# Kernel optimization log

Measured on AMD Instinct MI355X. Metric: run time of the kernel, lower is better.

## Reference

```python
import jax, jax.numpy as jnp
import numpy as np

B, N, D, H, C = 2048, 6, 2048, 1024, 200  # batch, nodes/graph, feat dim, hidden, classes
ALPHA = 0.015   # distance decay in edge weight
SCALE = 24.0    # weight rescale after mean-subtraction + clamp


def setup_inputs() -> dict:
    key = jax.random.key(0)
    k1, k2, k3, k4 = jax.random.split(key, 4)
    part_feats = jax.random.normal(k1, (B, N, D), dtype=jnp.float32)
    # cdds columns: [score, y0, x0, y1, x1, idx]; only cols 1:5 (box coords) are used
    cdds = jax.random.uniform(k2, (B, N, 6), dtype=jnp.float32) * 448.0
    fc_w = jax.random.normal(k3, (2 * D, H), dtype=jnp.float32) * 0.02
    fc_b = jnp.zeros((H,), dtype=jnp.float32)
    cls_w = jax.random.normal(k4, (H, C), dtype=jnp.float32) * 0.02
    cls_b = jnp.zeros((C,), dtype=jnp.float32)
    return {"part_feats": part_feats, "cdds": cdds, "fc_w": fc_w, "fc_b": fc_b,
            "cls_w": cls_w, "cls_b": cls_b}


def reference(part_feats, cdds, fc_w, fc_b, cls_w, cls_b):
    # --- edge weights on per-sample complete graph (apply_edges) ---
    loc = cdds[:, :, 1:5]                      # (B, N, 4) = (y0, x0, y1, x1)
    cy = (loc[..., 0] + loc[..., 2]) * 0.5     # node center y, (B, N)
    cx = (loc[..., 1] + loc[..., 3]) * 0.5     # node center x, (B, N)
    dx = cx[:, :, None] - cx[:, None, :]       # (B, N, N) pairwise
    dy = cy[:, :, None] - cy[:, None, :]
    d2 = dx * dx + dy * dy
    mask = ~jnp.eye(N, dtype=bool)             # off-diagonal = real edges (30 per graph)
    dist = jnp.sqrt(jnp.where(mask, d2, 1.0))  # safe sqrt off the diagonal
    w0 = jnp.where(mask, jnp.exp(-ALPHA * dist), 0.0)
    mean_w = jnp.sum(w0, axis=(1, 2), keepdims=True) / (N * (N - 1))  # mean over 30 edges
    w = SCALE * jnp.maximum(w0 - mean_w, 0.0) * mask                  # (B, N, N), w[b,u,v]
    # --- update_all: u_mul_e + mean over the (N-1) incoming edges per node ---
    hidden = jnp.einsum('buv,bud->bvd', w, part_feats) / (N - 1)      # (B, N, D)
    # --- node MLP + graph mean readout + classifier ---
    node_ft = jnp.concatenate([hidden, part_feats], axis=-1) @ fc_w + fc_b  # (B, N, H)
    g_ft = node_ft.mean(axis=1)                                             # (B, H)
    return g_ft @ cls_w + cls_b                                             # (B, C)
```

## Files before the change

kernel.cpp:

```cpp
#include <hip/hip_runtime.h>
#include <math.h>

namespace {
constexpr int NB = 2048;
constexpr int NNODE = 6;
constexpr int DD = 2048;
constexpr int HH = 1024;
constexpr int CC = 200;
constexpr int K2 = 2 * DD;
constexpr int NPAD = 256;
constexpr int ZS1 = 4;
constexpr int ZS2 = 16;
constexpr float ALPHA_C = 0.015f;
constexpr float SCALE_C = 24.0f;
}

typedef __attribute__((ext_vector_type(8))) short bf16x8;
typedef __attribute__((ext_vector_type(4))) float f32x4;

static __device__ __forceinline__ unsigned short f2bf(float x) {
    union { float f; unsigned int u; } v; v.f = x;
    unsigned int r = v.u + 0x7FFFu + ((v.u >> 16) & 1u);
    return (unsigned short)(r >> 16);
}

static __device__ __forceinline__ void compute_s_wave(const float* __restrict__ cdds,
                                                      int b, float sv[NNODE]) {
    const int lane = threadIdx.x & 63;
    const int u = lane >> 3;
    const int v = lane & 7;
    const float* cd = cdds + (size_t)b * 36;
    float w = 0.f;
    const bool valid = (u < 6) & (v < 6) & (u != v);
    if (u < 6 && v < 6 && u != v) {
        float cyu = (cd[u * 6 + 1] + cd[u * 6 + 3]) * 0.5f;
        float cxu = (cd[u * 6 + 2] + cd[u * 6 + 4]) * 0.5f;
        float cyv = (cd[v * 6 + 1] + cd[v * 6 + 3]) * 0.5f;
        float cxv = (cd[v * 6 + 2] + cd[v * 6 + 4]) * 0.5f;
        float dx = cxu - cxv, dy = cyu - cyv;
        w = expf(-ALPHA_C * sqrtf(dx * dx + dy * dy));
    }
    float s = w;
#pragma unroll
    for (int m = 32; m >= 1; m >>= 1) s += __shfl_xor(s, m);
    float mean = s * (1.f / 30.f);
    float tt = valid ? fmaxf(w - mean, 0.f) : 0.f;
    tt += __shfl_xor(tt, 1);
    tt += __shfl_xor(tt, 2);
    tt += __shfl_xor(tt, 4);
    float su = SCALE_C * tt * 0.2f;
#pragma unroll
    for (int uu = 0; uu < NNODE; ++uu) sv[uu] = __shfl(su, uu * 8);
}

__global__ __launch_bounds__(256) void k_cvt(const float* __restrict__ cls_w,
                                             unsigned short* __restrict__ cls_wT)
{
    __shared__ float sm[64 * 65];
    const int kt = blockIdx.x & 15;
    const int nt = blockIdx.x >> 4;
    const int t = threadIdx.x;
#pragma unroll
    for (int c = 0; c < 4; ++c) {
        int i = t + c * 256;
        int kr = i >> 4;
        int n4 = (i & 15) << 2;
        int gn = nt * 64 + n4;
        const float* sp = cls_w + (size_t)(kt * 64 + kr) * CC + gn;
        float4 v = {0.f, 0.f, 0.f, 0.f};
        if (gn + 3 < CC) {
            v = *(const float4*)sp;
        } else {
            if (gn + 0 < CC) v.x = sp[0];
            if (gn + 1 < CC) v.y = sp[1];
            if (gn + 2 < CC) v.z = sp[2];
            if (gn + 3 < CC) v.w = sp[3];
        }
        sm[kr * 65 + n4 + 0] = v.x; sm[kr * 65 + n4 + 1] = v.y;
        sm[kr * 65 + n4 + 2] = v.z; sm[kr * 65 + n4 + 3] = v.w;
    }
    __syncthreads();
#pragma unroll
    for (int c = 0; c < 4; ++c) {
        int i = t + c * 256;
        int nr = i >> 4;
        int k4 = (i & 15) << 2;
        ushort4 o;
        o.x = f2bf(sm[(k4 + 0) * 65 + nr]);
        o.y = f2bf(sm[(k4 + 1) * 65 + nr]);
        o.z = f2bf(sm[(k4 + 2) * 65 + nr]);
        o.w = f2bf(sm[(k4 + 3) * 65 + nr]);
        *(ushort4*)(cls_wT + (size_t)(nt * 64 + nr) * HH + kt * 64 + k4) = o;
    }
}

__global__ __launch_bounds__(256) void k_g1(const float* __restrict__ fc_w,
                                            const unsigned short* __restrict__ Bt,
                                            float* __restrict__ partM)
{
    __shared__ short As[32][72];
    __shared__ short Bs[256][72];
    const int t = threadIdx.x;
    const int lane = t & 63;
    const int wid = t >> 6;
    const int bm = blockIdx.x * 32;
    const int z = blockIdx.y;
    const int kbase = z * (HH / ZS1);

    f32x4 acc[2][4] = {};

    for (int k0 = kbase; k0 < kbase + HH / ZS1; k0 += 64) {
#pragma unroll
        for (int c = 0; c < 2; ++c) {
            int i = t + c * 256;
            int row = i >> 4;
            int k4 = (i & 15) << 2;
            float4 v = *(const float4*)(fc_w + (size_t)(bm + row) * HH + k0 + k4);
            ushort4 o;
            o.x = f2bf(v.x); o.y = f2bf(v.y); o.z = f2bf(v.z); o.w = f2bf(v.w);
            *(ushort4*)&As[row][k4] = o;
        }
#pragma unroll
        for (int c = 0; c < 8; ++c) {
            int i = t + c * 256;
            int n = i >> 3;
            int k8 = (i & 7) << 3;
            *(uint4*)&Bs[n][k8] =
                *(const uint4*)(Bt + (size_t)n * HH + k0 + k8);
        }
        __syncthreads();
#pragma unroll
        for (int ks = 0; ks < 2; ++ks) {
            int kk = ks * 32 + ((lane >> 4) << 3);
            int ar = lane & 15;
            bf16x8 a0 = *(const bf16x8*)&As[ar][kk];
            bf16x8 a1 = *(const bf16x8*)&As[16 + ar][kk];
#pragma unroll
            for (int fn = 0; fn < 4; ++fn) {
                bf16x8 b = *(const bf16x8*)&Bs[wid * 64 + fn * 16 + ar][kk];
                acc[0][fn] = __builtin_amdgcn_mfma_f32_16x16x32_bf16(a0, b, acc[0][fn], 0, 0, 0);
                acc[1][fn] = __builtin_amdgcn_mfma_f32_16x16x32_bf16(a1, b, acc[1][fn], 0, 0, 0);
            }
        }
        __syncthreads();
    }
#pragma unroll
    for (int fm = 0; fm < 2; ++fm)
#pragma unroll
        for (int fn = 0; fn < 4; ++fn) {
            int gm0 = bm + fm * 16 + ((lane >> 4) << 2);
            int gn = wid * 64 + fn * 16 + (lane & 15);
#pragma unroll
            for (int r = 0; r < 4; ++r)
                partM[((size_t)z * K2 + gm0 + r) * NPAD + gn] = acc[fm][fn][r];
        }
}

__global__ __launch_bounds__(256) void k_red(const float* __restrict__ partM,
                                             const float* __restrict__ cls_w,
                                             const float* __restrict__ fc_b,
                                             const float* __restrict__ cls_b,
                                             unsigned short* __restrict__ Mt,
                                             float* __restrict__ bvec)
{
    __shared__ float sm[64][69];
    __shared__ float red[256];
    const int bx = blockIdx.x;
    const int t = threadIdx.x;

    if (bx >= 256) {
        const int bb = bx - 256;
        int c8 = t & 7;
        int hs = t >> 3;
        int c = bb * 8 + c8;
        float acc = 0.f;
        for (int h = hs; h < HH; h += 32)
            acc += fc_b[h] * cls_w[(size_t)h * CC + c];
        red[t] = acc;
        __syncthreads();
        for (int s = 128; s >= 8; s >>= 1) {
            if (t < s) red[t] += red[t + s];
            __syncthreads();
        }
        if (t < 8) bvec[c] = red[t] + cls_b[c];
        return;
    }

    const int bm = (bx >> 2) * 64;
    const int bn = (bx & 3) * 64;
#pragma unroll
    for (int c = 0; c < 4; ++c) {
        int i = t + c * 256;
        int mr = i >> 4;
        int n4 = (i & 15) << 2;
        float4 s = {0.f, 0.f, 0.f, 0.f};
#pragma unroll
        for (int z = 0; z < ZS1; ++z) {
            float4 v = *(const float4*)(partM +
                ((size_t)z * K2 + bm + mr) * NPAD + bn + n4);
            s.x += v.x; s.y += v.y; s.z += v.z; s.w += v.w;
        }
        sm[mr][n4 + 0] = s.x; sm[mr][n4 + 1] = s.y;
        sm[mr][n4 + 2] = s.z; sm[mr][n4 + 3] = s.w;
    }
    __syncthreads();
#pragma unroll
    for (int c = 0; c < 4; ++c) {
        int i = t + c * 256;
        int nr = i >> 4;
        int m4 = (i & 15) << 2;
        ushort4 o;
        o.x = f2bf(sm[m4 + 0][nr]);
        o.y = f2bf(sm[m4 + 1][nr]);
        o.z = f2bf(sm[m4 + 2][nr]);
        o.w = f2bf(sm[m4 + 3][nr]);
        *(ushort4*)(Mt + (size_t)(bn + nr) * K2 + bm + m4) = o;
    }
}

__global__ __launch_bounds__(256) void k_pq(const float* __restrict__ pf,
                                            const float* __restrict__ cdds,
                                            unsigned short* __restrict__ pq)
{
    const int bid = blockIdx.x;
    const int b = bid >> 1;
    const int d = ((bid & 1) << 10) + (threadIdx.x << 2);

    const float* base = pf + (size_t)b * NNODE * DD + d;
    float4 v0 = *(const float4*)(base + 0 * DD);
    float4 v1 = *(const float4*)(base + 1 * DD);
    float4 v2 = *(const float4*)(base + 2 * DD);
    float4 v3 = *(const float4*)(base + 3 * DD);
    float4 v4 = *(const float4*)(base + 4 * DD);
    float4 v5 = *(const float4*)(base + 5 * DD);

    float sv[NNODE];
    compute_s_wave(cdds, b, sv);

    float4 q;
    q.x = v0.x + v1.x + v2.x + v3.x + v4.x + v5.x;
    q.y = v0.y + v1.y + v2.y + v3.y + v4.y + v5.y;
    q.z = v0.z + v1.z + v2.z + v3.z + v4.z + v5.z;
    q.w = v0.w + v1.w + v2.w + v3.w + v4.w + v5.w;

    float4 p = {0.f, 0.f, 0.f, 0.f};
    p.x = fmaf(sv[0], v0.x, p.x); p.y = fmaf(sv[0], v0.y, p.y);
    p.z = fmaf(sv[0], v0.z, p.z); p.w = fmaf(sv[0], v0.w, p.w);
    p.x = fmaf(sv[1], v1.x, p.x); p.y = fmaf(sv[1], v1.y, p.y);
    p.z = fmaf(sv[1], v1.z, p.z); p.w = fmaf(sv[1], v1.w, p.w);
    p.x = fmaf(sv[2], v2.x, p.x); p.y = fmaf(sv[2], v2.y, p.y);
    p.z = fmaf(sv[2], v2.z, p.z); p.w = fmaf(sv[2], v2.w, p.w);
    p.x = fmaf(sv[3], v3.x, p.x); p.y = fmaf(sv[3], v3.y, p.y);
    p.z = fmaf(sv[3], v3.z, p.z); p.w = fmaf(sv[3], v3.w, p.w);
    p.x = fmaf(sv[4], v4.x, p.x); p.y = fmaf(sv[4], v4.y, p.y);
    p.z = fmaf(sv[4], v4.z, p.z); p.w = fmaf(sv[4], v4.w, p.w);
    p.x = fmaf(sv[5], v5.x, p.x); p.y = fmaf(sv[5], v5.y, p.y);
    p.z = fmaf(sv[5], v5.z, p.z); p.w = fmaf(sv[5], v5.w, p.w);

    unsigned short* o = pq + (size_t)b * K2;
    ushort4 pb, qb;
    pb.x = f2bf(p.x); pb.y = f2bf(p.y); pb.z = f2bf(p.z); pb.w = f2bf(p.w);
    qb.x = f2bf(q.x); qb.y = f2bf(q.y); qb.z = f2bf(q.z); qb.w = f2bf(q.w);
    *(ushort4*)(o + d) = pb;
    *(ushort4*)(o + DD + d) = qb;
}

__global__ __launch_bounds__(256) void k_gemm2(const unsigned short* __restrict__ A,
                                               const unsigned short* __restrict__ Bt,
                                               float* __restrict__ part)
{
    __shared__ short As[64][72];
    __shared__ short Bs[256][72];
    const int t = threadIdx.x;
    const int lane = t & 63;
    const int wid = t >> 6;
    const int wr = wid >> 1, wc = wid & 1;
    const int bm = blockIdx.x * 64;
    const int z = blockIdx.y;
    const int kbase = z * (K2 / ZS2);

    f32x4 acc[2][8] = {};

    for (int k0 = kbase; k0 < kbase + K2 / ZS2; k0 += 64) {
#pragma unroll
        for (int c = 0; c < 2; ++c) {
            int i = t + c * 256;
            int row = i >> 3;
            int k8 = (i & 7) << 3;
            *(uint4*)&As[row][k8] =
                *(const uint4*)(A + (size_t)(bm + row) * K2 + k0 + k8);
        }
#pragma unroll
        for (int c = 0; c < 8; ++c) {
            int i = t + c * 256;
            int n = i >> 3;
            int k8 = (i & 7) << 3;
            *(uint4*)&Bs[n][k8] =
                *(const uint4*)(Bt + (size_t)n * K2 + k0 + k8);
        }
        __syncthreads();
#pragma unroll
        for (int ks = 0; ks < 2; ++ks) {
            int kk = ks * 32 + ((lane >> 4) << 3);
            int ar = lane & 15;
            bf16x8 a0 = *(const bf16x8*)&As[wr * 32 + ar][kk];
            bf16x8 a1 = *(const bf16x8*)&As[wr * 32 + 16 + ar][kk];
#pragma unroll
            for (int fn = 0; fn < 8; ++fn) {
                bf16x8 b = *(const bf16x8*)&Bs[wc * 128 + fn * 16 + ar][kk];
                acc[0][fn] = __builtin_amdgcn_mfma_f32_16x16x32_bf16(a0, b, acc[0][fn], 0, 0, 0);
                acc[1][fn] = __builtin_amdgcn_mfma_f32_16x16x32_bf16(a1, b, acc[1][fn], 0, 0, 0);
            }
        }
        __syncthreads();
    }
#pragma unroll
    for (int fm = 0; fm < 2; ++fm)
#pragma unroll
        for (int fn = 0; fn < 8; ++fn) {
            int gm0 = bm + wr * 32 + fm * 16 + ((lane >> 4) << 2);
            int gn = wc * 128 + fn * 16 + (lane & 15);
#pragma unroll
            for (int r = 0; r < 4; ++r)
                part[((size_t)z * NB + gm0 + r) * NPAD + gn] = acc[fm][fn][r];
        }
}

__global__ __launch_bounds__(256) void k_combine(const float* __restrict__ part,
                                                 const float* __restrict__ bvec,
                                                 float* __restrict__ out)
{
    int idx = blockIdx.x * blockDim.x + threadIdx.x;
    if (idx >= NB * CC) return;
    int b = idx / CC;
    int c = idx - b * CC;
    float s = 0.f;
#pragma unroll
    for (int z = 0; z < ZS2; ++z)
        s += part[((size_t)z * NB + b) * NPAD + c];
    out[idx] = s * (1.f / 6.f) + bvec[c];
}

extern "C" void kernel_launch(void* const* d_in, const int* in_sizes, int n_in,
                              void* d_out, int out_size, void* d_ws, size_t ws_size,
                              hipStream_t stream)
{
    const float* part_feats = (const float*)d_in[0];
    const float* cdds = (const float*)d_in[1];
    const float* fc_w = (const float*)d_in[2];
    const float* fc_b = (const float*)d_in[3];
    const float* cls_w = (const float*)d_in[4];
    const float* cls_b = (const float*)d_in[5];
    float* out = (float*)d_out;

    char* ws = (char*)d_ws;
    size_t off = 0;
    unsigned short* pq = (unsigned short*)(ws + off);     off += (size_t)NB * K2 * 2;
    unsigned short* Mt = (unsigned short*)(ws + off);     off += (size_t)NPAD * K2 * 2;
    unsigned short* cls_wT = (unsigned short*)(ws + off); off += (size_t)NPAD * HH * 2;
    float* partM = (float*)(ws + off);                    off += (size_t)ZS1 * K2 * NPAD * 4;
    float* part = (float*)(ws + off);                     off += (size_t)ZS2 * NB * NPAD * 4;
    float* bvec = (float*)(ws + off);                     off += 256 * 4;

    k_cvt<<<dim3(64), dim3(256), 0, stream>>>(cls_w, cls_wT);
    k_pq<<<dim3(NB * 2), dim3(256), 0, stream>>>(part_feats, cdds, pq);
    k_g1<<<dim3(K2 / 32, ZS1), dim3(256), 0, stream>>>(fc_w, cls_wT, partM);
    k_red<<<dim3(256 + 25), dim3(256), 0, stream>>>(partM, cls_w, fc_b, cls_b, Mt, bvec);
    k_gemm2<<<dim3(NB / 64, ZS2), dim3(256), 0, stream>>>(pq, Mt, part);
    k_combine<<<dim3((NB * CC + 255) / 256), dim3(256), 0, stream>>>(part, bvec, out);
}
```

Measured before the change: 69.33 us.

## Merge independent kernels, store split-K partials in bf16, retile gemm2 warps

Folds the bias-vector computation into the cls_w conversion kernel and runs the pq feature-reduction blocks in the same launch as the first GEMM. This cuts launch count and lets independent work overlap. The second GEMM's split-K partials are now stored as bf16 instead of fp32, halving that write/read traffic, and the combine kernel reads them vectorized four at a time. The gemm2 warp tiling changes from a 2x2 warp grid to four warps each covering all 64 rows by 64 columns, which reuses the A fragments across more MFMAs. Rounding each of 16 partials to bf16 adds accuracy error.

Measured after the change: 69.93 us. Within noise of the previous version (+0.9%).

```diff
diff --git a/kernel.cpp b/kernel.cpp
--- a/kernel.cpp
+++ b/kernel.cpp
@@ -13,6 +13,8 @@
 constexpr int ZS2 = 16;
 constexpr float ALPHA_C = 0.015f;
 constexpr float SCALE_C = 24.0f;
+
+constexpr int G1_BLOCKS = (K2 / 32) * ZS1;
 }
 
 typedef __attribute__((ext_vector_type(8))) short bf16x8;
@@ -22,6 +24,11 @@
     union { float f; unsigned int u; } v; v.f = x;
     unsigned int r = v.u + 0x7FFFu + ((v.u >> 16) & 1u);
     return (unsigned short)(r >> 16);
+}
+
+static __device__ __forceinline__ float bf2f(unsigned short u) {
+    union { unsigned int i; float f; } v; v.i = ((unsigned int)u) << 16;
+    return v.f;
 }
 
 static __device__ __forceinline__ void compute_s_wave(const float* __restrict__ cdds,
@@ -53,13 +60,35 @@
     for (int uu = 0; uu < NNODE; ++uu) sv[uu] = __shfl(su, uu * 8);
 }
 
-__global__ __launch_bounds__(256) void k_cvt(const float* __restrict__ cls_w,
-                                             unsigned short* __restrict__ cls_wT)
+__global__ __launch_bounds__(256) void k_small(const float* __restrict__ cls_w,
+                                               const float* __restrict__ fc_b,
+                                               const float* __restrict__ cls_b,
+                                               unsigned short* __restrict__ cls_wT,
+                                               float* __restrict__ bvec)
 {
     __shared__ float sm[64 * 65];
-    const int kt = blockIdx.x & 15;
-    const int nt = blockIdx.x >> 4;
+    const int bx = blockIdx.x;
     const int t = threadIdx.x;
+    if (bx >= 64) {
+        const int bb = bx - 64;
+        float* red = sm;
+        int c8 = t & 7;
+        int hs = t >> 3;
+        int c = bb * 8 + c8;
+        float acc = 0.f;
+        for (int h = hs; h < HH; h += 32)
+            acc += fc_b[h] * cls_w[(size_t)h * CC + c];
+        red[t] = acc;
+        __syncthreads();
+        for (int s = 128; s >= 8; s >>= 1) {
+            if (t < s) red[t] += red[t + s];
+            __syncthreads();
+        }
+        if (t < 8) bvec[c] = red[t] + cls_b[c];
+        return;
+    }
+    const int kt = bx & 15;
+    const int nt = bx >> 4;
 #pragma unroll
     for (int c = 0; c < 4; ++c) {
         int i = t + c * 256;
@@ -94,17 +123,66 @@
     }
 }
 
-__global__ __launch_bounds__(256) void k_g1(const float* __restrict__ fc_w,
-                                            const unsigned short* __restrict__ Bt,
-                                            float* __restrict__ partM)
+__global__ __launch_bounds__(256) void k_mid(const float* __restrict__ pf,
+                                             const float* __restrict__ cdds,
+                                             const float* __restrict__ fc_w,
+                                             const unsigned short* __restrict__ Bt,
+                                             unsigned short* __restrict__ pq,
+                                             float* __restrict__ partM)
 {
     __shared__ short As[32][72];
     __shared__ short Bs[256][72];
+    const int bx = blockIdx.x;
     const int t = threadIdx.x;
+
+    if (bx >= G1_BLOCKS) {
+        const int bid = bx - G1_BLOCKS;
+        const int b = bid >> 1;
+        const int d = ((bid & 1) << 10) + (t << 2);
+        const float* base = pf + (size_t)b * NNODE * DD + d;
+        float4 v0 = *(const float4*)(base + 0 * DD);
+        float4 v1 = *(const float4*)(base + 1 * DD);
+        float4 v2 = *(const float4*)(base + 2 * DD);
+        float4 v3 = *(const float4*)(base + 3 * DD);
+        float4 v4 = *(const float4*)(base + 4 * DD);
+        float4 v5 = *(const float4*)(base + 5 * DD);
+
+        float sv[NNODE];
+        compute_s_wave(cdds, b, sv);
+
+        float4 q;
+        q.x = v0.x + v1.x + v2.x + v3.x + v4.x + v5.x;
+        q.y = v0.y + v1.y + v2.y + v3.y + v4.y + v5.y;
+        q.z = v0.z + v1.z + v2.z + v3.z + v4.z + v5.z;
+        q.w = v0.w + v1.w + v2.w + v3.w + v4.w + v5.w;
+
+        float4 p = {0.f, 0.f, 0.f, 0.f};
+        p.x = fmaf(sv[0], v0.x, p.x); p.y = fmaf(sv[0], v0.y, p.y);
+        p.z = fmaf(sv[0], v0.z, p.z); p.w = fmaf(sv[0], v0.w, p.w);
+        p.x = fmaf(sv[1], v1.x, p.x); p.y = fmaf(sv[1], v1.y, p.y);
+        p.z = fmaf(sv[1], v1.z, p.z); p.w = fmaf(sv[1], v1.w, p.w);
+        p.x = fmaf(sv[2], v2.x, p.x); p.y = fmaf(sv[2], v2.y, p.y);
+        p.z = fmaf(sv[2], v2.z, p.z); p.w = fmaf(sv[2], v2.w, p.w);
+        p.x = fmaf(sv[3], v3.x, p.x); p.y = fmaf(sv[3], v3.y, p.y);
+        p.z = fmaf(sv[3], v3.z, p.z); p.w = fmaf(sv[3], v3.w, p.w);
+        p.x = fmaf(sv[4], v4.x, p.x); p.y = fmaf(sv[4], v4.y, p.y);
+        p.z = fmaf(sv[4], v4.z, p.z); p.w = fmaf(sv[4], v4.w, p.w);
+        p.x = fmaf(sv[5], v5.x, p.x); p.y = fmaf(sv[5], v5.y, p.y);
+        p.z = fmaf(sv[5], v5.z, p.z); p.w = fmaf(sv[5], v5.w, p.w);
+
+        unsigned short* o = pq + (size_t)b * K2;
+        ushort4 pb, qb;
+        pb.x = f2bf(p.x); pb.y = f2bf(p.y); pb.z = f2bf(p.z); pb.w = f2bf(p.w);
+        qb.x = f2bf(q.x); qb.y = f2bf(q.y); qb.z = f2bf(q.z); qb.w = f2bf(q.w);
+        *(ushort4*)(o + d) = pb;
+        *(ushort4*)(o + DD + d) = qb;
+        return;
+    }
+
     const int lane = t & 63;
     const int wid = t >> 6;
-    const int bm = blockIdx.x * 32;
-    const int z = blockIdx.y;
+    const int bm = (bx >> 2) * 32;
+    const int z = bx & 3;
     const int kbase = z * (HH / ZS1);
 
     f32x4 acc[2][4] = {};
@@ -157,35 +235,11 @@
 }
 
 __global__ __launch_bounds__(256) void k_red(const float* __restrict__ partM,
-                                             const float* __restrict__ cls_w,
-                                             const float* __restrict__ fc_b,
-                                             const float* __restrict__ cls_b,
-                                             unsigned short* __restrict__ Mt,
-                                             float* __restrict__ bvec)
+                                             unsigned short* __restrict__ Mt)
 {
     __shared__ float sm[64][69];
-    __shared__ float red[256];
     const int bx = blockIdx.x;
     const int t = threadIdx.x;
-
-    if (bx >= 256) {
-        const int bb = bx - 256;
-        int c8 = t & 7;
-        int hs = t >> 3;
-        int c = bb * 8 + c8;
-        float acc = 0.f;
-        for (int h = hs; h < HH; h += 32)
-            acc += fc_b[h] * cls_w[(size_t)h * CC + c];
-        red[t] = acc;
-        __syncthreads();
-        for (int s = 128; s >= 8; s >>= 1) {
-            if (t < s) red[t] += red[t + s];
-            __syncthreads();
-        }
-        if (t < 8) bvec[c] = red[t] + cls_b[c];
-        return;
-    }
-
     const int bm = (bx >> 2) * 64;
     const int bn = (bx & 3) * 64;
 #pragma unroll
@@ -218,68 +272,20 @@
     }
 }
 
-__global__ __launch_bounds__(256) void k_pq(const float* __restrict__ pf,
-                                            const float* __restrict__ cdds,
-                                            unsigned short* __restrict__ pq)
-{
-    const int bid = blockIdx.x;
-    const int b = bid >> 1;
-    const int d = ((bid & 1) << 10) + (threadIdx.x << 2);
-
-    const float* base = pf + (size_t)b * NNODE * DD + d;
-    float4 v0 = *(const float4*)(base + 0 * DD);
-    float4 v1 = *(const float4*)(base + 1 * DD);
-    float4 v2 = *(const float4*)(base + 2 * DD);
-    float4 v3 = *(const float4*)(base + 3 * DD);
-    float4 v4 = *(const float4*)(base + 4 * DD);
-    float4 v5 = *(const float4*)(base + 5 * DD);
-
-    float sv[NNODE];
-    compute_s_wave(cdds, b, sv);
-
-    float4 q;
-    q.x = v0.x + v1.x + v2.x + v3.x + v4.x + v5.x;
-    q.y = v0.y + v1.y + v2.y + v3.y + v4.y + v5.y;
-    q.z = v0.z + v1.z + v2.z + v3.z + v4.z + v5.z;
-    q.w = v0.w + v1.w + v2.w + v3.w + v4.w + v5.w;
-
-    float4 p = {0.f, 0.f, 0.f, 0.f};
-    p.x = fmaf(sv[0], v0.x, p.x); p.y = fmaf(sv[0], v0.y, p.y);
-    p.z = fmaf(sv[0], v0.z, p.z); p.w = fmaf(sv[0], v0.w, p.w);
-    p.x = fmaf(sv[1], v1.x, p.x); p.y = fmaf(sv[1], v1.y, p.y);
-    p.z = fmaf(sv[1], v1.z, p.z); p.w = fmaf(sv[1], v1.w, p.w);
-    p.x = fmaf(sv[2], v2.x, p.x); p.y = fmaf(sv[2], v2.y, p.y);
-    p.z = fmaf(sv[2], v2.z, p.z); p.w = fmaf(sv[2], v2.w, p.w);
-    p.x = fmaf(sv[3], v3.x, p.x); p.y = fmaf(sv[3], v3.y, p.y);
-    p.z = fmaf(sv[3], v3.z, p.z); p.w = fmaf(sv[3], v3.w, p.w);
-    p.x = fmaf(sv[4], v4.x, p.x); p.y = fmaf(sv[4], v4.y, p.y);
-    p.z = fmaf(sv[4], v4.z, p.z); p.w = fmaf(sv[4], v4.w, p.w);
-    p.x = fmaf(sv[5], v5.x, p.x); p.y = fmaf(sv[5], v5.y, p.y);
-    p.z = fmaf(sv[5], v5.z, p.z); p.w = fmaf(sv[5], v5.w, p.w);
-
-    unsigned short* o = pq + (size_t)b * K2;
-    ushort4 pb, qb;
-    pb.x = f2bf(p.x); pb.y = f2bf(p.y); pb.z = f2bf(p.z); pb.w = f2bf(p.w);
-    qb.x = f2bf(q.x); qb.y = f2bf(q.y); qb.z = f2bf(q.z); qb.w = f2bf(q.w);
-    *(ushort4*)(o + d) = pb;
-    *(ushort4*)(o + DD + d) = qb;
-}
-
 __global__ __launch_bounds__(256) void k_gemm2(const unsigned short* __restrict__ A,
                                                const unsigned short* __restrict__ Bt,
-                                               float* __restrict__ part)
+                                               unsigned short* __restrict__ part)
 {
     __shared__ short As[64][72];
     __shared__ short Bs[256][72];
     const int t = threadIdx.x;
     const int lane = t & 63;
     const int wid = t >> 6;
-    const int wr = wid >> 1, wc = wid & 1;
     const int bm = blockIdx.x * 64;
     const int z = blockIdx.y;
     const int kbase = z * (K2 / ZS2);
 
-    f32x4 acc[2][8] = {};
+    f32x4 acc[4][4] = {};
 
     for (int k0 = kbase; k0 < kbase + K2 / ZS2; k0 += 64) {
 #pragma unroll
@@ -303,42 +309,53 @@
         for (int ks = 0; ks < 2; ++ks) {
             int kk = ks * 32 + ((lane >> 4) << 3);
             int ar = lane & 15;
-            bf16x8 a0 = *(const bf16x8*)&As[wr * 32 + ar][kk];
-            bf16x8 a1 = *(const bf16x8*)&As[wr * 32 + 16 + ar][kk];
-#pragma unroll
-            for (int fn = 0; fn < 8; ++fn) {
-                bf16x8 b = *(const bf16x8*)&Bs[wc * 128 + fn * 16 + ar][kk];
+            bf16x8 a0 = *(const bf16x8*)&As[0 * 16 + ar][kk];
+            bf16x8 a1 = *(const bf16x8*)&As[1 * 16 + ar][kk];
+            bf16x8 a2 = *(const bf16x8*)&As[2 * 16 + ar][kk];
+            bf16x8 a3 = *(const bf16x8*)&As[3 * 16 + ar][kk];
+#pragma unroll
+            for (int fn = 0; fn < 4; ++fn) {
+                bf16x8 b = *(const bf16x8*)&Bs[wid * 64 + fn * 16 + ar][kk];
                 acc[0][fn] = __builtin_amdgcn_mfma_f32_16x16x32_bf16(a0, b, acc[0][fn], 0, 0, 0);
                 acc[1][fn] = __builtin_amdgcn_mfma_f32_16x16x32_bf16(a1, b, acc[1][fn], 0, 0, 0);
+                acc[2][fn] = __builtin_amdgcn_mfma_f32_16x16x32_bf16(a2, b, acc[2][fn], 0, 0, 0);
+                acc[3][fn] = __builtin_amdgcn_mfma_f32_16x16x32_bf16(a3, b, acc[3][fn], 0, 0, 0);
             }
         }
         __syncthreads();
     }
 #pragma unroll
-    for (int fm = 0; fm < 2; ++fm)
-#pragma unroll
-        for (int fn = 0; fn < 8; ++fn) {
-            int gm0 = bm + wr * 32 + fm * 16 + ((lane >> 4) << 2);
-            int gn = wc * 128 + fn * 16 + (lane & 15);
+    for (int fm = 0; fm < 4; ++fm)
+#pragma unroll
+        for (int fn = 0; fn < 4; ++fn) {
+            int gm0 = bm + fm * 16 + ((lane >> 4) << 2);
+            int gn = wid * 64 + fn * 16 + (lane & 15);
 #pragma unroll
             for (int r = 0; r < 4; ++r)
-                part[((size_t)z * NB + gm0 + r) * NPAD + gn] = acc[fm][fn][r];
-        }
-}
-
-__global__ __launch_bounds__(256) void k_combine(const float* __restrict__ part,
+                part[((size_t)z * NB + gm0 + r) * NPAD + gn] = f2bf(acc[fm][fn][r]);
+        }
+}
+
+__global__ __launch_bounds__(256) void k_combine(const unsigned short* __restrict__ part,
                                                  const float* __restrict__ bvec,
                                                  float* __restrict__ out)
 {
     int idx = blockIdx.x * blockDim.x + threadIdx.x;
-    if (idx >= NB * CC) return;
-    int b = idx / CC;
-    int c = idx - b * CC;
-    float s = 0.f;
-#pragma unroll
-    for (int z = 0; z < ZS2; ++z)
-        s += part[((size_t)z * NB + b) * NPAD + c];
-    out[idx] = s * (1.f / 6.f) + bvec[c];
+    if (idx >= NB * (CC / 4)) return;
+    int b = idx / (CC / 4);
+    int c0 = (idx - b * (CC / 4)) << 2;
+    float s0 = 0.f, s1 = 0.f, s2 = 0.f, s3 = 0.f;
+#pragma unroll
+    for (int z = 0; z < ZS2; ++z) {
+        ushort4 v = *(const ushort4*)(part + ((size_t)z * NB + b) * NPAD + c0);
+        s0 += bf2f(v.x); s1 += bf2f(v.y); s2 += bf2f(v.z); s3 += bf2f(v.w);
+    }
+    float4 o;
+    o.x = s0 * (1.f / 6.f) + bvec[c0 + 0];
+    o.y = s1 * (1.f / 6.f) + bvec[c0 + 1];
+    o.z = s2 * (1.f / 6.f) + bvec[c0 + 2];
+    o.w = s3 * (1.f / 6.f) + bvec[c0 + 3];
+    *(float4*)(out + (size_t)b * CC + c0) = o;
 }
 
 extern "C" void kernel_launch(void* const* d_in, const int* in_sizes, int n_in,
@@ -359,13 +376,13 @@
     unsigned short* Mt = (unsigned short*)(ws + off);     off += (size_t)NPAD * K2 * 2;
     unsigned short* cls_wT = (unsigned short*)(ws + off); off += (size_t)NPAD * HH * 2;
     float* partM = (float*)(ws + off);                    off += (size_t)ZS1 * K2 * NPAD * 4;
-    float* part = (float*)(ws + off);                     off += (size_t)ZS2 * NB * NPAD * 4;
+    unsigned short* part = (unsigned short*)(ws + off);   off += (size_t)ZS2 * NB * NPAD * 2;
     float* bvec = (float*)(ws + off);                     off += 256 * 4;
 
-    k_cvt<<<dim3(64), dim3(256), 0, stream>>>(cls_w, cls_wT);
-    k_pq<<<dim3(NB * 2), dim3(256), 0, stream>>>(part_feats, cdds, pq);
-    k_g1<<<dim3(K2 / 32, ZS1), dim3(256), 0, stream>>>(fc_w, cls_wT, partM);
-    k_red<<<dim3(256 + 25), dim3(256), 0, stream>>>(partM, cls_w, fc_b, cls_b, Mt, bvec);
+    k_small<<<dim3(64 + 25), dim3(256), 0, stream>>>(cls_w, fc_b, cls_b, cls_wT, bvec);
+    k_mid<<<dim3(G1_BLOCKS + NB * 2), dim3(256), 0, stream>>>(
+        part_feats, cdds, fc_w, cls_wT, pq, partM);
+    k_red<<<dim3(256), dim3(256), 0, stream>>>(partM, Mt);
     k_gemm2<<<dim3(NB / 64, ZS2), dim3(256), 0, stream>>>(pq, Mt, part);
-    k_combine<<<dim3((NB * CC + 255) / 256), dim3(256), 0, stream>>>(part, bvec, out);
-}
+    k_combine<<<dim3((NB * (CC / 4) + 255) / 256), dim3(256), 0, stream>>>(part, bvec, out);
+}
```
